# Kernel optimization log

Hardware: AMD Instinct MI355X
Metric: run time of the kernel (lower is better)

Reference implementation:

```python
import jax, jax.numpy as jnp
import numpy as np

N_NODES = 100000
N_EDGES = 1600000
N_ETYPES = 3
IN_FEATS = 128
HEADS = 4
OUT_FEATS = 16
EDGE_FEATS = 64
NEG_SLOPE = 0.2


def setup_inputs() -> dict:
    key = jax.random.key(0)
    ks = jax.random.split(key, 10)
    return {
        "x": jax.random.normal(ks[0], (N_NODES, IN_FEATS), jnp.float32),
        "W": jax.random.normal(ks[1], (IN_FEATS, HEADS * OUT_FEATS), jnp.float32) * 0.05,
        "W_e": jax.random.normal(ks[2], (EDGE_FEATS, HEADS * EDGE_FEATS), jnp.float32) * 0.05,
        "attn_l": jax.random.normal(ks[3], (HEADS, OUT_FEATS), jnp.float32) * 0.1,
        "attn_r": jax.random.normal(ks[4], (HEADS, OUT_FEATS), jnp.float32) * 0.1,
        "attn_e": jax.random.normal(ks[5], (HEADS, EDGE_FEATS), jnp.float32) * 0.1,
        "edge_emb": jax.random.normal(ks[6], (N_ETYPES, EDGE_FEATS), jnp.float32),
        "src": jax.random.randint(ks[7], (N_EDGES,), 0, N_NODES, jnp.int32),
        "dst": jax.random.randint(ks[8], (N_EDGES,), 0, N_NODES, jnp.int32),
        "etype": jax.random.randint(ks[9], (N_EDGES,), 0, N_ETYPES, jnp.int32),
    }


def reference(x, W, W_e, attn_l, attn_r, attn_e, edge_emb, src, dst, etype):
    N = x.shape[0]
    H, D = attn_l.shape
    # node projection: [N, H, D]
    feat = (x @ W).reshape(N, H, D)
    # per-node attention halves: [N, H]
    el = jnp.einsum("nhd,hd->nh", feat, attn_l)
    er = jnp.einsum("nhd,hd->nh", feat, attn_r)
    # per-etype edge term: [T, H]
    e_feat = (edge_emb @ W_e).reshape(edge_emb.shape[0], H, -1)
    ee = jnp.einsum("the,he->th", e_feat, attn_e)
    # per-edge pre-softmax score: [E, H]
    s = el[src] + er[dst] + ee[etype]
    s = jnp.where(s > 0, s, NEG_SLOPE * s)  # leaky_relu
    # edge softmax over incoming edges of each dst node (homogeneous graph)
    m = jax.ops.segment_max(s, dst, num_segments=N)
    e = jnp.exp(s - m[dst])
    z = jax.ops.segment_sum(e, dst, num_segments=N)
    a = e / z[dst]  # [E, H]
    # u_mul_e + sum aggregation: [N, H, D]
    msg = feat[src] * a[:, :, None]
    rst = jax.ops.segment_sum(msg, dst, num_segments=N)
    return rst, a
```

## Files before the change

### kernel.cpp

```cpp
#include <hip/hip_runtime.h>
#include <hip/hip_bf16.h>

#define N_NODES   100000
#define N_EDGES   1600000
#define N_ETYPES  3
#define IN_FEATS  128
#define HEADS     4
#define OUT_FEATS 16
#define EDGE_FEATS 64
#define HD        64
#define NEG_SLOPE 0.2f
#define MAXD_LDS  128

#define NBUCK     400
#define NPB       250
#define PBLK      400
#define EPB       4000

typedef short s16x8 __attribute__((ext_vector_type(8)));
typedef float f32x4 __attribute__((ext_vector_type(4)));

__device__ __forceinline__ short f2bs(float f) {
    __hip_bfloat16 h = __float2bfloat16(f);
    return *reinterpret_cast<short*>(&h);
}

__global__ __launch_bounds__(256) void wt_prep_kernel(
    const float* __restrict__ W, short* __restrict__ WTb)
{
    const int t = blockIdx.x * 256 + threadIdx.x;
    const int k = t >> 6, n = t & 63;
    WTb[n * IN_FEATS + k] = f2bs(W[t]);
}

#define XS_STRIDE 136
__global__ __launch_bounds__(256) void feat_el_er_kernel(
    const float* __restrict__ x,
    const short* __restrict__ WTb,
    const float* __restrict__ attn_l,
    const float* __restrict__ attn_r,
    __hip_bfloat16* __restrict__ featb,
    float* __restrict__ el,
    float* __restrict__ er)
{
    __shared__ short Xs[16 * XS_STRIDE];
    __shared__ short Ws[64 * XS_STRIDE];

    const int t = threadIdx.x;
    const int row0 = blockIdx.x * 16;
    {
        const int r = t >> 4, k0 = (t & 15) * 8;
        const float4* xg = (const float4*)(x + (size_t)(row0 + r) * IN_FEATS + k0);
        const float4 v0 = xg[0], v1 = xg[1];
        s16x8 p;
        p[0] = f2bs(v0.x); p[1] = f2bs(v0.y); p[2] = f2bs(v0.z); p[3] = f2bs(v0.w);
        p[4] = f2bs(v1.x); p[5] = f2bs(v1.y); p[6] = f2bs(v1.z); p[7] = f2bs(v1.w);
        *(s16x8*)&Xs[r * XS_STRIDE + k0] = p;
    }
    {
#pragma unroll
        for (int j = 0; j < 4; ++j) {
            const int u = t + 256 * j;
            const int r = u >> 4, c = (u & 15) * 8;
            *(s16x8*)&Ws[r * XS_STRIDE + c] = *(const s16x8*)(WTb + r * IN_FEATS + c);
        }
    }
    __syncthreads();

    const int w    = t >> 6;
    const int lane = t & 63;
    const int m    = lane & 15;
    const int q    = lane >> 4;

    f32x4 acc = {0.f, 0.f, 0.f, 0.f};
#pragma unroll
    for (int kb = 0; kb < 4; ++kb) {
        const s16x8 af = *(const s16x8*)&Xs[m * XS_STRIDE + kb * 32 + q * 8];
        const s16x8 bf = *(const s16x8*)&Ws[(w * 16 + m) * XS_STRIDE + kb * 32 + q * 8];
        acc = __builtin_amdgcn_mfma_f32_16x16x32_bf16(af, bf, acc, 0, 0, 0);
    }

    const float al = attn_l[w * OUT_FEATS + m];
    const float ar = attn_r[w * OUT_FEATS + m];
#pragma unroll
    for (int r = 0; r < 4; ++r) {
        const int row = row0 + q * 4 + r;
        featb[(size_t)row * HD + w * 16 + m] = __float2bfloat16(acc[r]);
        float cl = acc[r] * al;
        float cr = acc[r] * ar;
#pragma unroll
        for (int msk = 1; msk < 16; msk <<= 1) {
            cl += __shfl_xor(cl, msk, 64);
            cr += __shfl_xor(cr, msk, 64);
        }
        if (m == 0) {
            el[row * HEADS + w] = cl;
            er[row * HEADS + w] = cr;
        }
    }
}

__global__ __launch_bounds__(64) void ee_kernel(
    const float* __restrict__ edge_emb,
    const float* __restrict__ W_e,
    const float* __restrict__ attn_e,
    float* __restrict__ ee)
{
    const int b  = blockIdx.x;
    const int ty = b >> 2;
    const int h  = b & 3;
    const int e  = threadIdx.x;

    float ef = 0.f;
#pragma unroll
    for (int k = 0; k < EDGE_FEATS; ++k)
        ef += edge_emb[ty * EDGE_FEATS + k] *
              W_e[k * (HEADS * EDGE_FEATS) + h * EDGE_FEATS + e];
    float v = ef * attn_e[h * EDGE_FEATS + e];
#pragma unroll
    for (int m = 1; m < 64; m <<= 1) v += __shfl_xor(v, m, 64);
    if (e == 0) ee[ty * HEADS + h] = v;
}

__global__ __launch_bounds__(256) void bucket_hist_kernel(
    const int* __restrict__ dst, int* __restrict__ bhist)
{
    __shared__ int h[NBUCK];
    const int t = threadIdx.x, b = blockIdx.x;
    for (int j = t; j < NBUCK; j += 256) h[j] = 0;
    __syncthreads();
    const int e0 = b * EPB;
    for (int i = t; i < EPB; i += 256)
        atomicAdd(&h[dst[e0 + i] / NPB], 1);
    __syncthreads();
    for (int j = t; j < NBUCK; j += 256) bhist[b * NBUCK + j] = h[j];
}

__global__ __launch_bounds__(256) void bucket_scan1_kernel(
    int* __restrict__ bhist, int* __restrict__ btot)
{
    __shared__ int sh[PBLK];
    const int t = threadIdx.x, j = blockIdx.x;
    const int j0 = t, j1 = t + 256;
    int o0 = 0, o1 = 0;
    if (j0 < PBLK) { o0 = bhist[j0 * NBUCK + j]; sh[j0] = o0; }
    if (j1 < PBLK) { o1 = bhist[j1 * NBUCK + j]; sh[j1] = o1; }
    __syncthreads();
    for (int off = 1; off < PBLK; off <<= 1) {
        int v0 = (j0 >= off && j0 < PBLK) ? sh[j0 - off] : 0;
        int v1 = (j1 >= off && j1 < PBLK) ? sh[j1 - off] : 0;
        __syncthreads();
        if (j0 < PBLK) sh[j0] += v0;
        if (j1 < PBLK) sh[j1] += v1;
        __syncthreads();
    }
    if (j0 < PBLK) bhist[j0 * NBUCK + j] = sh[j0] - o0;
    if (j1 < PBLK) bhist[j1 * NBUCK + j] = sh[j1] - o1;
    if (t == 255) btot[j] = sh[PBLK - 1];
}

__global__ __launch_bounds__(512) void bucket_scan2_kernel(
    const int* __restrict__ btot, int* __restrict__ bbase)
{
    __shared__ int sh[NBUCK];
    const int t = threadIdx.x;
    int o = 0;
    if (t < NBUCK) { o = btot[t]; sh[t] = o; }
    __syncthreads();
    for (int off = 1; off < NBUCK; off <<= 1) {
        int v = (t >= off && t < NBUCK) ? sh[t - off] : 0;
        __syncthreads();
        if (t < NBUCK) sh[t] += v;
        __syncthreads();
    }
    if (t < NBUCK) bbase[t] = sh[t] - o;
    if (t == NBUCK - 1) bbase[NBUCK] = sh[t];
}

__global__ __launch_bounds__(256) void bucket_scatter_kernel(
    const int* __restrict__ src, const int* __restrict__ dst,
    const int* __restrict__ etype,
    const int* __restrict__ bhist, const int* __restrict__ bbase,
    int2* __restrict__ sc_bucket)
{
    __shared__ int cnt[NBUCK];
    const int t = threadIdx.x, b = blockIdx.x;
    for (int j = t; j < NBUCK; j += 256)
        cnt[j] = bbase[j] + bhist[b * NBUCK + j];
    __syncthreads();
    const int e0 = b * EPB;
    for (int i = t; i < EPB; i += 256) {
        const int e  = e0 + i;
        const int dn = dst[e];
        const int bu = dn / NPB;
        const int ld = dn - bu * NPB;
        const int slot = atomicAdd(&cnt[bu], 1);
        sc_bucket[slot] = make_int2(src[e], e | (etype[e] << 21) | (ld << 23));
    }
}

__global__ __launch_bounds__(256) void bucket_csr_kernel(
    const int2* __restrict__ sc_bucket, const int* __restrict__ bbase,
    int* __restrict__ ptr, int2* __restrict__ sc_csr)
{
    __shared__ int sdeg[256];
    __shared__ int scur[256];
    const int t = threadIdx.x, b = blockIdx.x;
    const int lo = bbase[b], hi = bbase[b + 1];
    const int count = hi - lo;

    sdeg[t] = 0;
    __syncthreads();
    for (int i = t; i < count; i += 256) {
        const int2 v = sc_bucket[lo + i];
        atomicAdd(&sdeg[(v.y >> 23) & 0xFF], 1);
    }
    __syncthreads();
    const int orig = sdeg[t];
    for (int off = 1; off < 256; off <<= 1) {
        const int v = (t >= off) ? sdeg[t - off] : 0;
        __syncthreads();
        sdeg[t] += v;
        __syncthreads();
    }
    const int excl = sdeg[t] - orig;
    if (t < NPB) ptr[b * NPB + t] = lo + excl;
    scur[t] = excl;
    if (b == 0 && t == 0) ptr[N_NODES] = N_EDGES;
    __syncthreads();
    for (int i = t; i < count; i += 256) {
        const int2 v = sc_bucket[lo + i];
        const int ld = (v.y >> 23) & 0xFF;
        const int slot = atomicAdd(&scur[ld], 1);
        sc_csr[lo + slot] = make_int2(v.x, (v.y & 0x1FFFFF) | (((v.y >> 21) & 3) << 24));
    }
}

__global__ __launch_bounds__(256) void agg_kernel(
    const int2* __restrict__ sc_csr, const int* __restrict__ ptr,
    const float* __restrict__ el, const float* __restrict__ er,
    const float* __restrict__ ee, const __hip_bfloat16* __restrict__ featb,
    float* __restrict__ rst, float* __restrict__ a_out)
{
    __shared__ float w_lds[4][MAXD_LDS * HEADS];
    const int wid  = threadIdx.x >> 6;
    const int lane = threadIdx.x & 63;
    const int n    = blockIdx.x * 4 + wid;

    const int p0  = ptr[n];
    const int deg = ptr[n + 1] - p0;
    float* wl = w_lds[wid];

    const int hA = lane & 3;
    const int eo = lane >> 2;
    const float er_nA = er[n * HEADS + hA];
    const float ee0 = ee[0 * HEADS + hA];
    const float ee1 = ee[1 * HEADS + hA];
    const float ee2 = ee[2 * HEADS + hA];
    float zacc = 0.f;
    const bool fast = (deg <= MAXD_LDS);
    for (int base = 0; base < deg; base += 16) {
        const int idx = base + eo;
        if (idx < deg) {
            const int2 sc = sc_csr[p0 + idx];
            const int ty = sc.y >> 24;
            const float eeh = (ty == 0) ? ee0 : ((ty == 1) ? ee1 : ee2);
            float s = el[sc.x * HEADS + hA] + er_nA + eeh;
            s = s > 0.f ? s : NEG_SLOPE * s;
            const float wv = __expf(s);
            if (fast) wl[idx * HEADS + hA] = wv;
            zacc += wv;
        }
    }
#pragma unroll
    for (int m = 4; m < 64; m <<= 1) zacc += __shfl_xor(zacc, m, 64);

    if (fast) {
        const int half  = lane >> 5;
        const int cpair = lane & 31;
        const int hB    = cpair >> 3;
        const float inv_z = (deg > 0) ? __frcp_rn(__shfl(zacc, hB, 64)) : 0.f;
        float rx = 0.f, ry = 0.f;
        int i = 0;
        for (; i + 4 <= deg; i += 4) {
            const int2 sc0 = sc_csr[p0 + i + half];
            const int2 sc1 = sc_csr[p0 + i + 2 + half];
            const uint f0 = *(const uint*)((const ushort*)featb + ((size_t)sc0.x << 6) + (cpair << 1));
            const uint f1 = *(const uint*)((const ushort*)featb + ((size_t)sc1.x << 6) + (cpair << 1));
            const float a0 = wl[(i + half) * HEADS + hB] * inv_z;
            const float a1 = wl[(i + 2 + half) * HEADS + hB] * inv_z;
            rx += __uint_as_float(f0 << 16) * a0;
            ry += __uint_as_float(f0 & 0xFFFF0000u) * a0;
            rx += __uint_as_float(f1 << 16) * a1;
            ry += __uint_as_float(f1 & 0xFFFF0000u) * a1;
            if ((lane & 7) == 0) {
                a_out[(size_t)(sc0.y & 0xFFFFFF) * HEADS + hB] = a0;
                a_out[(size_t)(sc1.y & 0xFFFFFF) * HEADS + hB] = a1;
            }
        }
        if (i + 2 <= deg) {
            const int2 sc0 = sc_csr[p0 + i + half];
            const uint f0 = *(const uint*)((const ushort*)featb + ((size_t)sc0.x << 6) + (cpair << 1));
            const float a0 = wl[(i + half) * HEADS + hB] * inv_z;
            rx += __uint_as_float(f0 << 16) * a0;
            ry += __uint_as_float(f0 & 0xFFFF0000u) * a0;
            if ((lane & 7) == 0)
                a_out[(size_t)(sc0.y & 0xFFFFFF) * HEADS + hB] = a0;
            i += 2;
        }
        if (i < deg) {
            const int2 sc0 = sc_csr[p0 + i];
            const uint f0 = *(const uint*)((const ushort*)featb + ((size_t)sc0.x << 6) + (cpair << 1));
            const float a0 = wl[i * HEADS + hB] * inv_z;
            if (half == 0) {
                rx += __uint_as_float(f0 << 16) * a0;
                ry += __uint_as_float(f0 & 0xFFFF0000u) * a0;
                if ((lane & 7) == 0)
                    a_out[(size_t)(sc0.y & 0xFFFFFF) * HEADS + hB] = a0;
            }
        }
        rx += __shfl_xor(rx, 32, 64);
        ry += __shfl_xor(ry, 32, 64);
        if (half == 0) {
            float2 v = make_float2(rx, ry);
            *(float2*)(rst + (size_t)n * HD + (cpair << 1)) = v;
        }
    } else {
        const int h = lane >> 4;
        const int d = lane & 15;
        const float inv_z = (deg > 0) ? __frcp_rn(__shfl(zacc, h, 64)) : 0.f;
        const float er_n = er[n * HEADS + h];
        const float g0 = ee[h], g1 = ee[HEADS + h], g2 = ee[2 * HEADS + h];
        float racc = 0.f;
        for (int i = 0; i < deg; ++i) {
            const int2 sc = sc_csr[p0 + i];
            const int ty = sc.y >> 24;
            const float eeh = (ty == 0) ? g0 : ((ty == 1) ? g1 : g2);
            float s = el[sc.x * HEADS + h] + er_n + eeh;
            s = s > 0.f ? s : NEG_SLOPE * s;
            const float a = __expf(s) * inv_z;
            racc += __bfloat162float(featb[(size_t)sc.x * HD + lane]) * a;
            if (d == 0) a_out[(size_t)(sc.y & 0xFFFFFF) * HEADS + h] = a;
        }
        rst[(size_t)n * HD + lane] = racc;
    }
}

extern "C" void kernel_launch(void* const* d_in, const int* in_sizes, int n_in,
                              void* d_out, int out_size, void* d_ws, size_t ws_size,
                              hipStream_t stream)
{
    const float* x        = (const float*)d_in[0];
    const float* W        = (const float*)d_in[1];
    const float* W_e      = (const float*)d_in[2];
    const float* attn_l   = (const float*)d_in[3];
    const float* attn_r   = (const float*)d_in[4];
    const float* attn_e   = (const float*)d_in[5];
    const float* edge_emb = (const float*)d_in[6];
    const int* src   = (const int*)d_in[7];
    const int* dst   = (const int*)d_in[8];
    const int* etype = (const int*)d_in[9];

    float* out     = (float*)d_out;
    float* rst_out = out;
    float* a_out   = out + (size_t)N_NODES * HD;

    char* w = (char*)d_ws;
    __hip_bfloat16* featb = (__hip_bfloat16*)w; w += (size_t)N_NODES * HD * 2;
    float* el    = (float*)w;  w += (size_t)N_NODES * HEADS * 4;
    float* er    = (float*)w;  w += (size_t)N_NODES * HEADS * 4;
    float* ee    = (float*)w;  w += 64;
    int*   ptr   = (int*)w;    w += (size_t)(N_NODES + 4) * 4;
    int*   bhist = (int*)w;    w += (size_t)PBLK * NBUCK * 4;
    int*   btot  = (int*)w;    w += (size_t)NBUCK * 4;
    int*   bbase = (int*)w;    w += (size_t)(NBUCK + 4) * 4;
    short* WTb   = (short*)w;  w += (size_t)HD * IN_FEATS * 2;
    int2*  sc_bucket = (int2*)w; w += (size_t)N_EDGES * 8;
    int2*  sc_csr    = (int2*)w; w += (size_t)N_EDGES * 8;

    wt_prep_kernel<<<(IN_FEATS * HD) / 256, 256, 0, stream>>>(W, WTb);
    feat_el_er_kernel<<<N_NODES / 16, 256, 0, stream>>>(
        x, WTb, attn_l, attn_r, featb, el, er);
    ee_kernel<<<N_ETYPES * HEADS, 64, 0, stream>>>(edge_emb, W_e, attn_e, ee);

    bucket_hist_kernel<<<PBLK, 256, 0, stream>>>(dst, bhist);
    bucket_scan1_kernel<<<NBUCK, 256, 0, stream>>>(bhist, btot);
    bucket_scan2_kernel<<<1, 512, 0, stream>>>(btot, bbase);
    bucket_scatter_kernel<<<PBLK, 256, 0, stream>>>(src, dst, etype, bhist, bbase, sc_bucket);
    bucket_csr_kernel<<<NBUCK, 256, 0, stream>>>(sc_bucket, bbase, ptr, sc_csr);

    agg_kernel<<<N_NODES / 4, 256, 0, stream>>>(
        sc_csr, ptr, el, er, ee, featb, rst_out, a_out);
}
```

Before: 304.3 us.

## Fuse softmax score pass into aggregation loop and stage CSR buckets in LDS

The aggregation kernel now computes attention scores, exp weights and the weighted feature sum in one pass over incoming edges, accumulating the denominator alongside and normalising at the end. The separate score-only pre-pass is dropped, and the attention outputs are written in a separate coalesced loop over the LDS-stored weights. The bucket-to-CSR pass uses twice as many smaller buckets and caches each bucket in shared memory so the input is read from global memory once instead of twice. Costs include more redundant el lookups and exp per lane, a larger scan over 800 buckets, and higher LDS use that may lower occupancy.

```diff
diff --git a/kernel.cpp b/kernel.cpp
--- a/kernel.cpp
+++ b/kernel.cpp
@@ -12,10 +12,11 @@
 #define NEG_SLOPE 0.2f
 #define MAXD_LDS  128
 
-#define NBUCK     400
-#define NPB       250
+#define NBUCK     800
+#define NPB       125
 #define PBLK      400
 #define EPB       4000
+#define BCAP      2560
 
 typedef short s16x8 __attribute__((ext_vector_type(8)));
 typedef float f32x4 __attribute__((ext_vector_type(4)));
@@ -159,7 +160,7 @@
     if (t == 255) btot[j] = sh[PBLK - 1];
 }
 
-__global__ __launch_bounds__(512) void bucket_scan2_kernel(
+__global__ __launch_bounds__(1024) void bucket_scan2_kernel(
     const int* __restrict__ btot, int* __restrict__ bbase)
 {
     __shared__ int sh[NBUCK];
@@ -203,36 +204,55 @@
     const int2* __restrict__ sc_bucket, const int* __restrict__ bbase,
     int* __restrict__ ptr, int2* __restrict__ sc_csr)
 {
-    __shared__ int sdeg[256];
-    __shared__ int scur[256];
+    __shared__ int2 sbuf[BCAP];
+    __shared__ int sdeg[128];
+    __shared__ int scur[128];
     const int t = threadIdx.x, b = blockIdx.x;
-    const int lo = bbase[b], hi = bbase[b + 1];
-    const int count = hi - lo;
-
-    sdeg[t] = 0;
-    __syncthreads();
-    for (int i = t; i < count; i += 256) {
-        const int2 v = sc_bucket[lo + i];
-        atomicAdd(&sdeg[(v.y >> 23) & 0xFF], 1);
-    }
-    __syncthreads();
-    const int orig = sdeg[t];
-    for (int off = 1; off < 256; off <<= 1) {
-        const int v = (t >= off) ? sdeg[t - off] : 0;
-        __syncthreads();
-        sdeg[t] += v;
-        __syncthreads();
-    }
-    const int excl = sdeg[t] - orig;
-    if (t < NPB) ptr[b * NPB + t] = lo + excl;
-    scur[t] = excl;
+    const int lo = bbase[b];
+    const int count = bbase[b + 1] - lo;
+    const bool staged = (count <= BCAP);
+
+    if (t < 128) sdeg[t] = 0;
+    __syncthreads();
+    if (staged) {
+        for (int i = t; i < count; i += 256) {
+            const int2 v = sc_bucket[lo + i];
+            sbuf[i] = v;
+            atomicAdd(&sdeg[(v.y >> 23) & 0x7F], 1);
+        }
+    } else {
+        for (int i = t; i < count; i += 256)
+            atomicAdd(&sdeg[(sc_bucket[lo + i].y >> 23) & 0x7F], 1);
+    }
+    __syncthreads();
+    const int orig = (t < 128) ? sdeg[t] : 0;
+    for (int off = 1; off < 128; off <<= 1) {
+        const int v = (t < 128 && t >= off) ? sdeg[t - off] : 0;
+        __syncthreads();
+        if (t < 128) sdeg[t] += v;
+        __syncthreads();
+    }
+    if (t < 128) {
+        const int excl = sdeg[t] - orig;
+        if (t < NPB) ptr[b * NPB + t] = lo + excl;
+        scur[t] = lo + excl;
+    }
     if (b == 0 && t == 0) ptr[N_NODES] = N_EDGES;
     __syncthreads();
-    for (int i = t; i < count; i += 256) {
-        const int2 v = sc_bucket[lo + i];
-        const int ld = (v.y >> 23) & 0xFF;
-        const int slot = atomicAdd(&scur[ld], 1);
-        sc_csr[lo + slot] = make_int2(v.x, (v.y & 0x1FFFFF) | (((v.y >> 21) & 3) << 24));
+    if (staged) {
+        for (int i = t; i < count; i += 256) {
+            const int2 v = sbuf[i];
+            const int ld = (v.y >> 23) & 0x7F;
+            const int slot = atomicAdd(&scur[ld], 1);
+            sc_csr[slot] = make_int2(v.x, (v.y & 0x1FFFFF) | (((v.y >> 21) & 3) << 24));
+        }
+    } else {
+        for (int i = t; i < count; i += 256) {
+            const int2 v = sc_bucket[lo + i];
+            const int ld = (v.y >> 23) & 0x7F;
+            const int slot = atomicAdd(&scur[ld], 1);
+            sc_csr[slot] = make_int2(v.x, (v.y & 0x1FFFFF) | (((v.y >> 21) & 3) << 24));
+        }
     }
 }
 
@@ -250,93 +270,116 @@
     const int p0  = ptr[n];
     const int deg = ptr[n + 1] - p0;
     float* wl = w_lds[wid];
-
-    const int hA = lane & 3;
-    const int eo = lane >> 2;
-    const float er_nA = er[n * HEADS + hA];
-    const float ee0 = ee[0 * HEADS + hA];
-    const float ee1 = ee[1 * HEADS + hA];
-    const float ee2 = ee[2 * HEADS + hA];
-    float zacc = 0.f;
-    const bool fast = (deg <= MAXD_LDS);
-    for (int base = 0; base < deg; base += 16) {
-        const int idx = base + eo;
-        if (idx < deg) {
-            const int2 sc = sc_csr[p0 + idx];
-            const int ty = sc.y >> 24;
-            const float eeh = (ty == 0) ? ee0 : ((ty == 1) ? ee1 : ee2);
-            float s = el[sc.x * HEADS + hA] + er_nA + eeh;
-            s = s > 0.f ? s : NEG_SLOPE * s;
-            const float wv = __expf(s);
-            if (fast) wl[idx * HEADS + hA] = wv;
-            zacc += wv;
-        }
-    }
-#pragma unroll
-    for (int m = 4; m < 64; m <<= 1) zacc += __shfl_xor(zacc, m, 64);
-
-    if (fast) {
+    const ushort* fb = (const ushort*)featb;
+
+    if (deg <= MAXD_LDS) {
         const int half  = lane >> 5;
         const int cpair = lane & 31;
         const int hB    = cpair >> 3;
-        const float inv_z = (deg > 0) ? __frcp_rn(__shfl(zacc, hB, 64)) : 0.f;
-        float rx = 0.f, ry = 0.f;
+        const bool accL = (cpair & 7) == 0;
+        const float er_n = er[n * HEADS + hB];
+        const float g0 = ee[hB], g1 = ee[HEADS + hB], g2 = ee[2 * HEADS + hB];
+
+        float zacc = 0.f, rx = 0.f, ry = 0.f;
         int i = 0;
         for (; i + 4 <= deg; i += 4) {
             const int2 sc0 = sc_csr[p0 + i + half];
             const int2 sc1 = sc_csr[p0 + i + 2 + half];
-            const uint f0 = *(const uint*)((const ushort*)featb + ((size_t)sc0.x << 6) + (cpair << 1));
-            const uint f1 = *(const uint*)((const ushort*)featb + ((size_t)sc1.x << 6) + (cpair << 1));
-            const float a0 = wl[(i + half) * HEADS + hB] * inv_z;
-            const float a1 = wl[(i + 2 + half) * HEADS + hB] * inv_z;
-            rx += __uint_as_float(f0 << 16) * a0;
-            ry += __uint_as_float(f0 & 0xFFFF0000u) * a0;
-            rx += __uint_as_float(f1 << 16) * a1;
-            ry += __uint_as_float(f1 & 0xFFFF0000u) * a1;
-            if ((lane & 7) == 0) {
-                a_out[(size_t)(sc0.y & 0xFFFFFF) * HEADS + hB] = a0;
-                a_out[(size_t)(sc1.y & 0xFFFFFF) * HEADS + hB] = a1;
+            const uint f0 = *(const uint*)(fb + ((size_t)sc0.x << 6) + (cpair << 1));
+            const uint f1 = *(const uint*)(fb + ((size_t)sc1.x << 6) + (cpair << 1));
+            const float el0 = el[sc0.x * HEADS + hB];
+            const float el1 = el[sc1.x * HEADS + hB];
+            const int ty0 = sc0.y >> 24, ty1 = sc1.y >> 24;
+            float s0 = el0 + er_n + ((ty0 == 0) ? g0 : ((ty0 == 1) ? g1 : g2));
+            float s1 = el1 + er_n + ((ty1 == 0) ? g0 : ((ty1 == 1) ? g1 : g2));
+            s0 = s0 > 0.f ? s0 : NEG_SLOPE * s0;
+            s1 = s1 > 0.f ? s1 : NEG_SLOPE * s1;
+            const float w0 = __expf(s0), w1 = __expf(s1);
+            if (accL) {
+                zacc += w0 + w1;
+                wl[(i + half) * HEADS + hB]     = w0;
+                wl[(i + 2 + half) * HEADS + hB] = w1;
             }
+            rx += __uint_as_float(f0 << 16) * w0 + __uint_as_float(f1 << 16) * w1;
+            ry += __uint_as_float(f0 & 0xFFFF0000u) * w0 + __uint_as_float(f1 & 0xFFFF0000u) * w1;
         }
         if (i + 2 <= deg) {
             const int2 sc0 = sc_csr[p0 + i + half];
-            const uint f0 = *(const uint*)((const ushort*)featb + ((size_t)sc0.x << 6) + (cpair << 1));
-            const float a0 = wl[(i + half) * HEADS + hB] * inv_z;
-            rx += __uint_as_float(f0 << 16) * a0;
-            ry += __uint_as_float(f0 & 0xFFFF0000u) * a0;
-            if ((lane & 7) == 0)
-                a_out[(size_t)(sc0.y & 0xFFFFFF) * HEADS + hB] = a0;
+            const uint f0 = *(const uint*)(fb + ((size_t)sc0.x << 6) + (cpair << 1));
+            const float el0 = el[sc0.x * HEADS + hB];
+            const int ty0 = sc0.y >> 24;
+            float s0 = el0 + er_n + ((ty0 == 0) ? g0 : ((ty0 == 1) ? g1 : g2));
+            s0 = s0 > 0.f ? s0 : NEG_SLOPE * s0;
+            const float w0 = __expf(s0);
+            if (accL) {
+                zacc += w0;
+                wl[(i + half) * HEADS + hB] = w0;
+            }
+            rx += __uint_as_float(f0 << 16) * w0;
+            ry += __uint_as_float(f0 & 0xFFFF0000u) * w0;
             i += 2;
         }
         if (i < deg) {
-            const int2 sc0 = sc_csr[p0 + i];
-            const uint f0 = *(const uint*)((const ushort*)featb + ((size_t)sc0.x << 6) + (cpair << 1));
-            const float a0 = wl[i * HEADS + hB] * inv_z;
             if (half == 0) {
-                rx += __uint_as_float(f0 << 16) * a0;
-                ry += __uint_as_float(f0 & 0xFFFF0000u) * a0;
-                if ((lane & 7) == 0)
-                    a_out[(size_t)(sc0.y & 0xFFFFFF) * HEADS + hB] = a0;
+                const int2 sc0 = sc_csr[p0 + i];
+                const uint f0 = *(const uint*)(fb + ((size_t)sc0.x << 6) + (cpair << 1));
+                const float el0 = el[sc0.x * HEADS + hB];
+                const int ty0 = sc0.y >> 24;
+                float s0 = el0 + er_n + ((ty0 == 0) ? g0 : ((ty0 == 1) ? g1 : g2));
+                s0 = s0 > 0.f ? s0 : NEG_SLOPE * s0;
+                const float w0 = __expf(s0);
+                if (accL) {
+                    zacc += w0;
+                    wl[i * HEADS + hB] = w0;
+                }
+                rx += __uint_as_float(f0 << 16) * w0;
+                ry += __uint_as_float(f0 & 0xFFFF0000u) * w0;
             }
         }
+        zacc += __shfl_xor(zacc, 32, 64);
+        const float inv_z = (deg > 0) ? __frcp_rn(__shfl(zacc, hB << 3, 64)) : 0.f;
+
         rx += __shfl_xor(rx, 32, 64);
         ry += __shfl_xor(ry, 32, 64);
         if (half == 0) {
-            float2 v = make_float2(rx, ry);
+            float2 v = make_float2(rx * inv_z, ry * inv_z);
             *(float2*)(rst + (size_t)n * HD + (cpair << 1)) = v;
         }
+        const int hA = lane & 3;
+        const int eo = lane >> 2;
+        const float inv_zA = (deg > 0) ? __frcp_rn(__shfl(zacc, hA << 3, 64)) : 0.f;
+        for (int idx = eo; idx < deg; idx += 16) {
+            const int ey = sc_csr[p0 + idx].y & 0xFFFFFF;
+            a_out[(size_t)ey * HEADS + hA] = wl[idx * HEADS + hA] * inv_zA;
+        }
     } else {
+        const int hA = lane & 3;
+        const int eo = lane >> 2;
+        const float er_nA = er[n * HEADS + hA];
+        const float a0 = ee[hA], a1 = ee[HEADS + hA], a2 = ee[2 * HEADS + hA];
+        float zacc = 0.f;
+        for (int base = 0; base < deg; base += 16) {
+            const int idx = base + eo;
+            if (idx < deg) {
+                const int2 sc = sc_csr[p0 + idx];
+                const int ty = sc.y >> 24;
+                float s = el[sc.x * HEADS + hA] + er_nA + ((ty == 0) ? a0 : ((ty == 1) ? a1 : a2));
+                s = s > 0.f ? s : NEG_SLOPE * s;
+                zacc += __expf(s);
+            }
+        }
+#pragma unroll
+        for (int m = 4; m < 64; m <<= 1) zacc += __shfl_xor(zacc, m, 64);
         const int h = lane >> 4;
         const int d = lane & 15;
-        const float inv_z = (deg > 0) ? __frcp_rn(__shfl(zacc, h, 64)) : 0.f;
+        const float inv_z = __frcp_rn(__shfl(zacc, h, 64));
         const float er_n = er[n * HEADS + h];
         const float g0 = ee[h], g1 = ee[HEADS + h], g2 = ee[2 * HEADS + h];
         float racc = 0.f;
         for (int i = 0; i < deg; ++i) {
             const int2 sc = sc_csr[p0 + i];
             const int ty = sc.y >> 24;
-            const float eeh = (ty == 0) ? g0 : ((ty == 1) ? g1 : g2);
-            float s = el[sc.x * HEADS + h] + er_n + eeh;
+            float s = el[sc.x * HEADS + h] + er_n + ((ty == 0) ? g0 : ((ty == 1) ? g1 : g2));
             s = s > 0.f ? s : NEG_SLOPE * s;
             const float a = __expf(s) * inv_z;
             racc += __bfloat162float(featb[(size_t)sc.x * HD + lane]) * a;
@@ -385,7 +428,7 @@
 
     bucket_hist_kernel<<<PBLK, 256, 0, stream>>>(dst, bhist);
     bucket_scan1_kernel<<<NBUCK, 256, 0, stream>>>(bhist, btot);
-    bucket_scan2_kernel<<<1, 512, 0, stream>>>(btot, bbase);
+    bucket_scan2_kernel<<<1, 1024, 0, stream>>>(btot, bbase);
     bucket_scatter_kernel<<<PBLK, 256, 0, stream>>>(src, dst, etype, bhist, bbase, sc_bucket);
     bucket_csr_kernel<<<NBUCK, 256, 0, stream>>>(sc_bucket, bbase, ptr, sc_csr);
 
```

New measurement: 290.6 us. -4.5%, faster.
